# Kernel tuning notes

Hardware: AMD Instinct MI355X
Metric: run time of the kernel (lower is better)

## Reference

```python
import jax, jax.numpy as jnp
import numpy as np

N = 100000
E = 1600000


def gcn_conv(x, W, b, src, dst, n):
    # PyG GCNConv: h = x @ W, symmetric normalization with self-loops, then + b
    h = x @ W  # [N, out]
    ones = jnp.ones(src.shape, dtype=h.dtype)
    deg = jax.ops.segment_sum(ones, dst, num_segments=n)  # in-degree incl self-loops
    dinv = jnp.where(deg > 0, jax.lax.rsqrt(deg), 0.0)
    norm = dinv[src] * dinv[dst]  # [E]
    msg = h[src] * norm[:, None]  # gather + scale
    out = jax.ops.segment_sum(msg, dst, num_segments=n)  # scatter-add
    return out + b


def setup_inputs() -> dict:
    key = jax.random.key(0)
    k1, k2, k3, k4 = jax.random.split(key, 4)
    x = jax.random.normal(k1, (N, 128), dtype=jnp.float32)
    edge_index = jax.random.randint(k2, (2, E), 0, N, dtype=jnp.int64)
    # Glorot-ish init for weights
    W1 = jax.random.normal(k3, (128, 64), dtype=jnp.float32) / np.sqrt(128.0)
    b1 = jnp.zeros((64,), dtype=jnp.float32)
    W2 = jax.random.normal(k4, (64, 64), dtype=jnp.float32) / np.sqrt(64.0)
    b2 = jnp.zeros((64,), dtype=jnp.float32)
    return {"x": x, "edge_index": edge_index, "W1": W1, "b1": b1, "W2": W2, "b2": b2}


def reference(x, edge_index, W1, b1, W2, b2):
    n = x.shape[0]
    loops = jnp.arange(n, dtype=edge_index.dtype)
    src = jnp.concatenate([edge_index[0], loops])  # add self-loops (GCNConv default)
    dst = jnp.concatenate([edge_index[1], loops])
    h = jax.nn.relu(gcn_conv(x, W1, b1, src, dst, n))
    out = gcn_conv(h, W2, b2, src, dst, n)
    return out
```

## Files before the change

kernel.cpp:

```cpp
#include <hip/hip_runtime.h>


#define GSB 2048

__global__ __launch_bounds__(256) void detect_dtype_kernel(const unsigned* __restrict__ w,
                                                           int E, unsigned* __restrict__ flag) {
  __shared__ unsigned sacc;
  if (threadIdx.x == 0) sacc = 0u;
  __syncthreads();
  int ns = min(16384, E);
  unsigned acc = 0;
  for (int i = threadIdx.x; i < ns; i += 256) acc |= w[2 * i + 1];
  if (__any(acc != 0) && (threadIdx.x & 63) == 0) sacc = 1u;
  __syncthreads();
  if (threadIdx.x == 0) *flag = sacc;
}

__global__ void convert_edges_kernel(const int* __restrict__ w, int E,
                                     const unsigned* __restrict__ flag,
                                     int* __restrict__ src32, int* __restrict__ dst32,
                                     int* __restrict__ cnt) {
  bool is64 = (*flag == 0u);
  int stride = gridDim.x * blockDim.x;
  for (int e = blockIdx.x * blockDim.x + threadIdx.x; e < E; e += stride) {
    int s, d;
    if (is64) {
      s = w[2 * (long)e];
      d = w[2 * ((long)E + e)];
    } else {
      s = w[e];
      d = w[(long)E + e];
    }
    src32[e] = s;
    dst32[e] = d;
    atomicAdd(&cnt[d], 1);
  }
}

#define SCAN_BS 256
__global__ void scan_block_kernel(const int* __restrict__ cnt, int n, int* __restrict__ bsums) {
  __shared__ int s[SCAN_BS];
  int gid = blockIdx.x * SCAN_BS + threadIdx.x;
  s[threadIdx.x] = (gid < n) ? cnt[gid] : 0;
  __syncthreads();
  for (int st = SCAN_BS / 2; st > 0; st >>= 1) {
    if (threadIdx.x < st) s[threadIdx.x] += s[threadIdx.x + st];
    __syncthreads();
  }
  if (threadIdx.x == 0) bsums[blockIdx.x] = s[0];
}

__global__ __launch_bounds__(512) void scan_bsums_kernel(int* __restrict__ bsums, int nb) {
  __shared__ int s[512];
  int carry = 0;
  for (int base = 0; base < nb; base += 512) {
    int g = base + threadIdx.x;
    int v = (g < nb) ? bsums[g] : 0;
    s[threadIdx.x] = v;
    __syncthreads();
    for (int st = 1; st < 512; st <<= 1) {
      int t = (threadIdx.x >= st) ? s[threadIdx.x - st] : 0;
      __syncthreads();
      s[threadIdx.x] += t;
      __syncthreads();
    }
    if (g < nb) bsums[g] = carry + s[threadIdx.x] - v;
    carry += s[511];
    __syncthreads();
  }
}

__global__ void scan_apply_kernel(const int* __restrict__ cnt, int n,
                                  const int* __restrict__ bsums, int* __restrict__ offs,
                                  float* __restrict__ dinv, int E) {
  __shared__ int s[SCAN_BS];
  int gid = blockIdx.x * SCAN_BS + threadIdx.x;
  int v = (gid < n) ? cnt[gid] : 0;
  s[threadIdx.x] = v;
  __syncthreads();
  for (int st = 1; st < SCAN_BS; st <<= 1) {
    int t = (threadIdx.x >= st) ? s[threadIdx.x - st] : 0;
    __syncthreads();
    s[threadIdx.x] += t;
    __syncthreads();
  }
  if (gid < n) {
    offs[gid] = bsums[blockIdx.x] + s[threadIdx.x] - v;
    dinv[gid] = rsqrtf((float)v + 1.0f);
    if (gid == n - 1) offs[n] = E;
  }
}

__global__ void build_csr_kernel(const int* __restrict__ src, const int* __restrict__ dst, int E,
                                 const int* __restrict__ offs, int* __restrict__ fill,
                                 const float* __restrict__ dinv,
                                 int* __restrict__ csrc, float* __restrict__ cnorm) {
  int stride = gridDim.x * blockDim.x;
  for (int e = blockIdx.x * blockDim.x + threadIdx.x; e < E; e += stride) {
    int s = src[e], d = dst[e];
    int pos = offs[d] + atomicAdd(&fill[d], 1);
    csrc[pos] = s;
    cnorm[pos] = dinv[s] * dinv[d];
  }
}

template <int K>
__global__ __launch_bounds__(256) void gemm_kernel(const float* __restrict__ X,
                                                   const float* __restrict__ W,
                                                   float* __restrict__ H, int n) {
  __shared__ float Ws[K * 64];
  for (int i = threadIdx.x; i < K * 64; i += 256) Ws[i] = W[i];
  __syncthreads();
  int row = blockIdx.x * 256 + threadIdx.x;
  if (row >= n) return;
  const float4* xr = (const float4*)(X + (size_t)row * K);
  float acc[64];
#pragma unroll
  for (int c = 0; c < 64; c++) acc[c] = 0.f;
#pragma unroll 4
  for (int k4 = 0; k4 < K / 4; k4++) {
    float4 xv = xr[k4];
#pragma unroll
    for (int kk = 0; kk < 4; kk++) {
      float xs = (kk == 0) ? xv.x : (kk == 1) ? xv.y : (kk == 2) ? xv.z : xv.w;
      const float4* wr = (const float4*)&Ws[(k4 * 4 + kk) * 64];
#pragma unroll
      for (int c4 = 0; c4 < 16; c4++) {
        float4 wv = wr[c4];
        acc[c4 * 4 + 0] += xs * wv.x;
        acc[c4 * 4 + 1] += xs * wv.y;
        acc[c4 * 4 + 2] += xs * wv.z;
        acc[c4 * 4 + 3] += xs * wv.w;
      }
    }
  }
  float4* ho = (float4*)(H + (size_t)row * 64);
#pragma unroll
  for (int c4 = 0; c4 < 16; c4++) {
    float4 v;
    v.x = acc[c4 * 4 + 0]; v.y = acc[c4 * 4 + 1];
    v.z = acc[c4 * 4 + 2]; v.w = acc[c4 * 4 + 3];
    ho[c4] = v;
  }
}

__global__ __launch_bounds__(256) void aggregate_kernel(
    const float* __restrict__ H, const int* __restrict__ offs,
    const int* __restrict__ csrc, const float* __restrict__ cnorm,
    const float* __restrict__ dinv, const float* __restrict__ bias,
    float* __restrict__ OUT, int n, int relu) {
  int wid = (blockIdx.x * 256 + threadIdx.x) >> 6;
  int lane = threadIdx.x & 63;
  if (wid >= n) return;
  float bv = bias[lane];
  float di = dinv[wid];
  int beg = offs[wid];
  int end = offs[wid + 1];
  float acc = H[(size_t)wid * 64 + lane] * (di * di);
  for (int base = beg; base < end; base += 64) {
    int m = min(64, end - base);
    int sl = 0; float nl = 0.f;
    if (lane < m) { sl = csrc[base + lane]; nl = cnorm[base + lane]; }
    int mr = (m + 15) & ~15;
    for (int j = 0; j < mr; j += 16) {
      int s[16]; float w[16]; float h[16];
#pragma unroll
      for (int t = 0; t < 16; t++) {
        s[t] = __shfl(sl, j + t);
        w[t] = __shfl(nl, j + t);
      }
#pragma unroll
      for (int t = 0; t < 16; t++) h[t] = H[(size_t)s[t] * 64 + lane];
#pragma unroll
      for (int t = 0; t < 16; t++) acc += h[t] * w[t];
    }
  }
  acc += bv;
  if (relu) acc = fmaxf(acc, 0.f);
  OUT[(size_t)wid * 64 + lane] = acc;
}

extern "C" void kernel_launch(void* const* d_in, const int* in_sizes, int n_in,
                              void* d_out, int out_size, void* d_ws, size_t ws_size,
                              hipStream_t stream) {
  const float* x  = (const float*)d_in[0];
  const int*   ei = (const int*)d_in[1];
  const float* W1 = (const float*)d_in[2];
  const float* b1 = (const float*)d_in[3];
  const float* W2 = (const float*)d_in[4];
  const float* b2 = (const float*)d_in[5];
  float* out = (float*)d_out;

  const int N = in_sizes[0] / 128;
  const int E = in_sizes[1] / 2;

  size_t off = 0;
  char* base = (char*)d_ws;
  auto alloc = [&](size_t bytes) -> void* {
    void* p = base + off;
    off += (bytes + 255) & ~(size_t)255;
    return p;
  };
  int*      cnt  = (int*)alloc((size_t)N * 4);
  int*      fill = (int*)alloc((size_t)N * 4);
  unsigned* flag = (unsigned*)alloc(256);
  size_t zero_bytes = off;
  int*   offs  = (int*)alloc((size_t)(N + 1) * 4);
  float* dinv  = (float*)alloc((size_t)N * 4);
  int nb = (N + SCAN_BS - 1) / SCAN_BS;
  int*   bsums = (int*)alloc((size_t)nb * 4);
  int*   src32 = (int*)alloc((size_t)E * 4);
  int*   dst32 = (int*)alloc((size_t)E * 4);
  int*   csrc  = (int*)alloc((size_t)E * 4);
  float* cnorm = (float*)alloc((size_t)E * 4);
  float* h1    = (float*)alloc((size_t)N * 64 * 4);
  float* a1    = (float*)alloc((size_t)N * 64 * 4);
  float* h2    = h1;

  hipMemsetAsync(d_ws, 0, zero_bytes, stream);

  detect_dtype_kernel<<<1, 256, 0, stream>>>((const unsigned*)ei, E, flag);
  convert_edges_kernel<<<GSB, 256, 0, stream>>>(ei, E, flag, src32, dst32, cnt);
  scan_block_kernel<<<nb, SCAN_BS, 0, stream>>>(cnt, N, bsums);
  scan_bsums_kernel<<<1, 512, 0, stream>>>(bsums, nb);
  scan_apply_kernel<<<nb, SCAN_BS, 0, stream>>>(cnt, N, bsums, offs, dinv, E);
  build_csr_kernel<<<GSB, 256, 0, stream>>>(src32, dst32, E, offs, fill, dinv, csrc, cnorm);

  gemm_kernel<128><<<(N + 255) / 256, 256, 0, stream>>>(x, W1, h1, N);
  aggregate_kernel<<<(N + 3) / 4, 256, 0, stream>>>(h1, offs, csrc, cnorm, dinv, b1, a1, N, 1);

  gemm_kernel<64><<<(N + 255) / 256, 256, 0, stream>>>(a1, W2, h2, N);
  aggregate_kernel<<<(N + 3) / 4, 256, 0, stream>>>(h2, offs, csrc, cnorm, dinv, b2, out, N, 0);
}
```

Before: 443.7 us.

## Fuse degree count with first GEMM, drop edge conversion, pack CSR records

Merges the degree-counting pass and the first GEMM into one launch, with the block index choosing which work a block does, so the atomics and the dense GEMM can overlap. Drops the intermediate src32/dst32 arrays: the CSR build now reads the raw edge_index directly. CSR source index and norm are interleaved into int2 records so the aggregate kernel issues one 8-byte load per edge instead of two. The edge index is read twice from the original int64 layout, and the fused kernel carries 32KB of shared memory even in its counting blocks, which may lower occupancy for those blocks.

```diff
diff --git a/kernel.cpp b/kernel.cpp
--- a/kernel.cpp
+++ b/kernel.cpp
@@ -16,24 +16,58 @@
   if (threadIdx.x == 0) *flag = sacc;
 }
 
-__global__ void convert_edges_kernel(const int* __restrict__ w, int E,
-                                     const unsigned* __restrict__ flag,
-                                     int* __restrict__ src32, int* __restrict__ dst32,
-                                     int* __restrict__ cnt) {
-  bool is64 = (*flag == 0u);
-  int stride = gridDim.x * blockDim.x;
-  for (int e = blockIdx.x * blockDim.x + threadIdx.x; e < E; e += stride) {
-    int s, d;
-    if (is64) {
-      s = w[2 * (long)e];
-      d = w[2 * ((long)E + e)];
-    } else {
-      s = w[e];
-      d = w[(long)E + e];
-    }
-    src32[e] = s;
-    dst32[e] = d;
-    atomicAdd(&cnt[d], 1);
+__device__ __forceinline__ int edge_src(const int* w, long e, long E, bool is64) {
+  return is64 ? w[2 * e] : w[e];
+}
+__device__ __forceinline__ int edge_dst(const int* w, long e, long E, bool is64) {
+  return is64 ? w[2 * (E + e)] : w[E + e];
+}
+
+__global__ __launch_bounds__(256) void count_gemm1_kernel(
+    const int* __restrict__ w, int E, const unsigned* __restrict__ flag,
+    int* __restrict__ cnt,
+    const float* __restrict__ X, const float* __restrict__ W,
+    float* __restrict__ H, int n) {
+  if (blockIdx.x < GSB) {
+    bool is64 = (*flag == 0u);
+    int stride = GSB * 256;
+    for (int e = blockIdx.x * 256 + threadIdx.x; e < E; e += stride)
+      atomicAdd(&cnt[edge_dst(w, e, E, is64)], 1);
+    return;
+  }
+  __shared__ float Ws[128 * 64];
+  for (int i = threadIdx.x; i < 128 * 64; i += 256) Ws[i] = W[i];
+  __syncthreads();
+  int row = (blockIdx.x - GSB) * 256 + threadIdx.x;
+  if (row >= n) return;
+  const float4* xr = (const float4*)(X + (size_t)row * 128);
+  float acc[64];
+#pragma unroll
+  for (int c = 0; c < 64; c++) acc[c] = 0.f;
+#pragma unroll 4
+  for (int k4 = 0; k4 < 32; k4++) {
+    float4 xv = xr[k4];
+#pragma unroll
+    for (int kk = 0; kk < 4; kk++) {
+      float xs = (kk == 0) ? xv.x : (kk == 1) ? xv.y : (kk == 2) ? xv.z : xv.w;
+      const float4* wr = (const float4*)&Ws[(k4 * 4 + kk) * 64];
+#pragma unroll
+      for (int c4 = 0; c4 < 16; c4++) {
+        float4 wv = wr[c4];
+        acc[c4 * 4 + 0] += xs * wv.x;
+        acc[c4 * 4 + 1] += xs * wv.y;
+        acc[c4 * 4 + 2] += xs * wv.z;
+        acc[c4 * 4 + 3] += xs * wv.w;
+      }
+    }
+  }
+  float4* ho = (float4*)(H + (size_t)row * 64);
+#pragma unroll
+  for (int c4 = 0; c4 < 16; c4++) {
+    float4 v;
+    v.x = acc[c4 * 4 + 0]; v.y = acc[c4 * 4 + 1];
+    v.z = acc[c4 * 4 + 2]; v.w = acc[c4 * 4 + 3];
+    ho[c4] = v;
   }
 }
 
@@ -91,62 +125,27 @@
   }
 }
 
-__global__ void build_csr_kernel(const int* __restrict__ src, const int* __restrict__ dst, int E,
+__global__ void build_csr_kernel(const int* __restrict__ w, int E,
+                                 const unsigned* __restrict__ flag,
                                  const int* __restrict__ offs, int* __restrict__ fill,
                                  const float* __restrict__ dinv,
-                                 int* __restrict__ csrc, float* __restrict__ cnorm) {
+                                 int2* __restrict__ csr) {
+  bool is64 = (*flag == 0u);
   int stride = gridDim.x * blockDim.x;
   for (int e = blockIdx.x * blockDim.x + threadIdx.x; e < E; e += stride) {
-    int s = src[e], d = dst[e];
+    int s = edge_src(w, e, E, is64);
+    int d = edge_dst(w, e, E, is64);
     int pos = offs[d] + atomicAdd(&fill[d], 1);
-    csrc[pos] = s;
-    cnorm[pos] = dinv[s] * dinv[d];
-  }
-}
-
-template <int K>
-__global__ __launch_bounds__(256) void gemm_kernel(const float* __restrict__ X,
-                                                   const float* __restrict__ W,
-                                                   float* __restrict__ H, int n) {
-  __shared__ float Ws[K * 64];
-  for (int i = threadIdx.x; i < K * 64; i += 256) Ws[i] = W[i];
-  __syncthreads();
-  int row = blockIdx.x * 256 + threadIdx.x;
-  if (row >= n) return;
-  const float4* xr = (const float4*)(X + (size_t)row * K);
-  float acc[64];
-#pragma unroll
-  for (int c = 0; c < 64; c++) acc[c] = 0.f;
-#pragma unroll 4
-  for (int k4 = 0; k4 < K / 4; k4++) {
-    float4 xv = xr[k4];
-#pragma unroll
-    for (int kk = 0; kk < 4; kk++) {
-      float xs = (kk == 0) ? xv.x : (kk == 1) ? xv.y : (kk == 2) ? xv.z : xv.w;
-      const float4* wr = (const float4*)&Ws[(k4 * 4 + kk) * 64];
-#pragma unroll
-      for (int c4 = 0; c4 < 16; c4++) {
-        float4 wv = wr[c4];
-        acc[c4 * 4 + 0] += xs * wv.x;
-        acc[c4 * 4 + 1] += xs * wv.y;
-        acc[c4 * 4 + 2] += xs * wv.z;
-        acc[c4 * 4 + 3] += xs * wv.w;
-      }
-    }
-  }
-  float4* ho = (float4*)(H + (size_t)row * 64);
-#pragma unroll
-  for (int c4 = 0; c4 < 16; c4++) {
-    float4 v;
-    v.x = acc[c4 * 4 + 0]; v.y = acc[c4 * 4 + 1];
-    v.z = acc[c4 * 4 + 2]; v.w = acc[c4 * 4 + 3];
-    ho[c4] = v;
+    int2 rec;
+    rec.x = s;
+    rec.y = __float_as_int(dinv[s] * dinv[d]);
+    csr[pos] = rec;
   }
 }
 
 __global__ __launch_bounds__(256) void aggregate_kernel(
     const float* __restrict__ H, const int* __restrict__ offs,
-    const int* __restrict__ csrc, const float* __restrict__ cnorm,
+    const int2* __restrict__ csr,
     const float* __restrict__ dinv, const float* __restrict__ bias,
     float* __restrict__ OUT, int n, int relu) {
   int wid = (blockIdx.x * 256 + threadIdx.x) >> 6;
@@ -160,7 +159,11 @@
   for (int base = beg; base < end; base += 64) {
     int m = min(64, end - base);
     int sl = 0; float nl = 0.f;
-    if (lane < m) { sl = csrc[base + lane]; nl = cnorm[base + lane]; }
+    if (lane < m) {
+      int2 rec = csr[base + lane];
+      sl = rec.x;
+      nl = __int_as_float(rec.y);
+    }
     int mr = (m + 15) & ~15;
     for (int j = 0; j < mr; j += 16) {
       int s[16]; float w[16]; float h[16];
@@ -178,6 +181,45 @@
   acc += bv;
   if (relu) acc = fmaxf(acc, 0.f);
   OUT[(size_t)wid * 64 + lane] = acc;
+}
+
+__global__ __launch_bounds__(256) void gemm2_kernel(const float* __restrict__ X,
+                                                    const float* __restrict__ W,
+                                                    float* __restrict__ H, int n) {
+  __shared__ float Ws[64 * 64];
+  for (int i = threadIdx.x; i < 64 * 64; i += 256) Ws[i] = W[i];
+  __syncthreads();
+  int row = blockIdx.x * 256 + threadIdx.x;
+  if (row >= n) return;
+  const float4* xr = (const float4*)(X + (size_t)row * 64);
+  float acc[64];
+#pragma unroll
+  for (int c = 0; c < 64; c++) acc[c] = 0.f;
+#pragma unroll 4
+  for (int k4 = 0; k4 < 16; k4++) {
+    float4 xv = xr[k4];
+#pragma unroll
+    for (int kk = 0; kk < 4; kk++) {
+      float xs = (kk == 0) ? xv.x : (kk == 1) ? xv.y : (kk == 2) ? xv.z : xv.w;
+      const float4* wr = (const float4*)&Ws[(k4 * 4 + kk) * 64];
+#pragma unroll
+      for (int c4 = 0; c4 < 16; c4++) {
+        float4 wv = wr[c4];
+        acc[c4 * 4 + 0] += xs * wv.x;
+        acc[c4 * 4 + 1] += xs * wv.y;
+        acc[c4 * 4 + 2] += xs * wv.z;
+        acc[c4 * 4 + 3] += xs * wv.w;
+      }
+    }
+  }
+  float4* ho = (float4*)(H + (size_t)row * 64);
+#pragma unroll
+  for (int c4 = 0; c4 < 16; c4++) {
+    float4 v;
+    v.x = acc[c4 * 4 + 0]; v.y = acc[c4 * 4 + 1];
+    v.z = acc[c4 * 4 + 2]; v.w = acc[c4 * 4 + 3];
+    ho[c4] = v;
+  }
 }
 
 extern "C" void kernel_launch(void* const* d_in, const int* in_sizes, int n_in,
@@ -209,26 +251,24 @@
   float* dinv  = (float*)alloc((size_t)N * 4);
   int nb = (N + SCAN_BS - 1) / SCAN_BS;
   int*   bsums = (int*)alloc((size_t)nb * 4);
-  int*   src32 = (int*)alloc((size_t)E * 4);
-  int*   dst32 = (int*)alloc((size_t)E * 4);
-  int*   csrc  = (int*)alloc((size_t)E * 4);
-  float* cnorm = (float*)alloc((size_t)E * 4);
+  int2*  csr   = (int2*)alloc((size_t)E * 8);
   float* h1    = (float*)alloc((size_t)N * 64 * 4);
   float* a1    = (float*)alloc((size_t)N * 64 * 4);
   float* h2    = h1;
 
   hipMemsetAsync(d_ws, 0, zero_bytes, stream);
 
+  int gemm_blocks = (N + 255) / 256;
+
   detect_dtype_kernel<<<1, 256, 0, stream>>>((const unsigned*)ei, E, flag);
-  convert_edges_kernel<<<GSB, 256, 0, stream>>>(ei, E, flag, src32, dst32, cnt);
+  count_gemm1_kernel<<<GSB + gemm_blocks, 256, 0, stream>>>(ei, E, flag, cnt, x, W1, h1, N);
   scan_block_kernel<<<nb, SCAN_BS, 0, stream>>>(cnt, N, bsums);
   scan_bsums_kernel<<<1, 512, 0, stream>>>(bsums, nb);
   scan_apply_kernel<<<nb, SCAN_BS, 0, stream>>>(cnt, N, bsums, offs, dinv, E);
-  build_csr_kernel<<<GSB, 256, 0, stream>>>(src32, dst32, E, offs, fill, dinv, csrc, cnorm);
-
-  gemm_kernel<128><<<(N + 255) / 256, 256, 0, stream>>>(x, W1, h1, N);
-  aggregate_kernel<<<(N + 3) / 4, 256, 0, stream>>>(h1, offs, csrc, cnorm, dinv, b1, a1, N, 1);
-
-  gemm_kernel<64><<<(N + 255) / 256, 256, 0, stream>>>(a1, W2, h2, N);
-  aggregate_kernel<<<(N + 3) / 4, 256, 0, stream>>>(h2, offs, csrc, cnorm, dinv, b2, out, N, 0);
-}
+  build_csr_kernel<<<GSB, 256, 0, stream>>>(ei, E, flag, offs, fill, dinv, csr);
+
+  aggregate_kernel<<<(N + 3) / 4, 256, 0, stream>>>(h1, offs, csr, dinv, b1, a1, N, 1);
+
+  gemm2_kernel<<<gemm_blocks, 256, 0, stream>>>(a1, W2, h2, N);
+  aggregate_kernel<<<(N + 3) / 4, 256, 0, stream>>>(h2, offs, csr, dinv, b2, out, N, 0);
+}
```

After: 446.0 us. No clear change (+0.5%).
